# Kernel tuning notes

Measured on AMD Instinct MI355X. Metric: run time of the kernel, lower is better.

The kernel has to match this reference:

```python
import jax, jax.numpy as jnp
import numpy as np

HOLE_P = 0.05      # fraction of NaN (invalid) pixels
N_PROP = 8         # fixed propagation iterations for hole filling
DOWN_LIMIT = 512   # original code downsamples masks when max dim > 512

# cv2.getStructuringElement(cv2.MORPH_ELLIPSE, (3,3)) is the 4-neighbor cross
_CROSS = np.array([[0., 1., 0.], [1., 1., 1.], [0., 1., 0.]], np.float32)


def _conv_cross_hw(x):
    """3x3 cross conv on a single [H, W] map, zero padding."""
    k = jnp.asarray(_CROSS)[None, None]  # [1,1,3,3]
    y = jax.lax.conv_general_dilated(x[None, None], k, (1, 1), 'SAME',
                                     dimension_numbers=('NCHW', 'OIHW', 'NCHW'))
    return y[0, 0]


def _conv_cross_chw(x):
    """Depthwise 3x3 cross conv on [C, H, W], zero padding."""
    c = x.shape[0]
    k = jnp.tile(jnp.asarray(_CROSS)[None, None], (c, 1, 1, 1))  # [C,1,3,3]
    y = jax.lax.conv_general_dilated(x[None], k, (1, 1), 'SAME',
                                     feature_group_count=c,
                                     dimension_numbers=('NCHW', 'OIHW', 'NCHW'))
    return y[0]


def _dilated_union_mask(invalid_f):
    """Replicates the tri-branch: F.conv2d with weight [1,C,3,3] sums over
    channels (union of per-class invalid masks), then clamps to [0,1].
    When max dim > 512 it nearest-downsamples by dr, dilates, and nearest-
    upsamples back. invalid_f: [C,H,W] float -> [H,W] float in {0,1}."""
    c, h, w = invalid_f.shape
    s = invalid_f.sum(0)  # channel sum == conv over channel dim
    m = max(c, h, w)
    if m > DOWN_LIMIT:
        dr = m / DOWN_LIMIT
        hs, ws = int(h / dr), int(w / dr)
        # nearest downsample: index floor(i * h / hs)
        ri = (jnp.arange(hs) * h // hs).astype(jnp.int32)
        ci = (jnp.arange(ws) * w // ws).astype(jnp.int32)
        s_small = s[ri][:, ci]
        d_small = jnp.clip(_conv_cross_hw(s_small), 0.0, 1.0)
        # nearest upsample back to (h, w)
        ri_up = (jnp.arange(h) * hs // h).astype(jnp.int32)
        ci_up = (jnp.arange(w) * ws // w).astype(jnp.int32)
        d = d_small[ri_up][:, ci_up]
    else:
        d = jnp.clip(_conv_cross_hw(s), 0.0, 1.0)
    return d


def _fill_missing(x, invalid):
    """NaN-free formulation of fillMissingValues_tensor (tri mode).
    x: [C,H,W] float values; invalid: [C,H,W] bool (pixels that were NaN).
    Source pixels = valid pixels adjacent to the dilated union invalid mask
    (plus the 4 image corners, as in the original corner fixup). Invalid
    pixels are filled by iterative 4-neighbor weighted propagation from the
    source set (GPU-native stand-in for the Interp2D triangulated fill)."""
    invalid_f = invalid.astype(jnp.float32)
    dil = _dilated_union_mask(invalid_f)                       # [H,W]
    src = (dil[None] * (1.0 - invalid_f))                      # [C,H,W]
    # corner fixup: *0 then +1 -> forced to 1
    for (i, j) in [(0, 0), (0, -1), (-1, 0), (-1, -1)]:
        src = src.at[:, i, j].set(1.0)
    v = jnp.where(src > 0, jnp.where(invalid, 0.0, x), 0.0)
    w = jnp.where(src > 0, 1.0, 0.0)

    def step(carry, _):
        v, w = carry
        nv = _conv_cross_chw(v)
        nw = _conv_cross_chw(w)
        new = (w == 0.0) & (nw > 0.0)
        v = jnp.where(new, nv / jnp.maximum(nw, 1e-6), v)
        w = jnp.where(new, 1.0, w)
        return (v, w), None

    (v, w), _ = jax.lax.scan(step, (v, w), None, length=N_PROP)
    # replace only the invalid pixels (original keeps valid pixels untouched)
    return jnp.where(invalid, v, x)


def setup_inputs() -> dict:
    key = jax.random.key(0)
    k1, k2 = jax.random.split(key)
    x = jax.random.normal(k1, (16, 1024, 1024), dtype=jnp.float32)
    hole_u = jax.random.uniform(k2, (16, 1024, 1024), dtype=jnp.float32)
    return {"x": x, "hole_u": hole_u}


def reference(x, hole_u):
    invalid = hole_u < HOLE_P  # models torch.isnan(target_for_interp)
    return _fill_missing(x, invalid)
```

## Files before the change

### kernel.cpp

```cpp
#include <hip/hip_runtime.h>

#define HOLE_P 0.05f
#define TW 64
#define TH 64
#define HALO 8
#define PRW 88
#define PRH 82
#define PLN 7216
#define PWORDS 1804
#define QCAP 1536

__global__ void k_mask(const float* __restrict__ hole_u, unsigned char* __restrict__ inv_mask) {
    int t = blockIdx.x * blockDim.x + threadIdx.x;
    const float* base = hole_u + (size_t)t * 8;
    float4 a = *reinterpret_cast<const float4*>(base);
    float4 b = *reinterpret_cast<const float4*>(base + 4);
    unsigned int m = (a.x < HOLE_P ? 1u : 0u)  | (a.y < HOLE_P ? 2u : 0u)  |
                     (a.z < HOLE_P ? 4u : 0u)  | (a.w < HOLE_P ? 8u : 0u)  |
                     (b.x < HOLE_P ? 16u : 0u) | (b.y < HOLE_P ? 32u : 0u) |
                     (b.z < HOLE_P ? 64u : 0u) | (b.w < HOLE_P ? 128u : 0u);
    inv_mask[t] = (unsigned char)m;
}

__global__ void k_us(const unsigned char* __restrict__ inv_mask, unsigned char* __restrict__ u_small) {
    int t = blockIdx.x * blockDim.x + threadIdx.x;
    int i  = t >> 7;
    int jb = t & 127;
    const unsigned char* p = inv_mask + (i << 8) + jb;
    unsigned int b = 0;
#pragma unroll
    for (int c = 0; c < 16; ++c) b |= p[c * 131072];
    unsigned int o = (b & 1u) | (((b >> 2) & 1u) << 8) | (((b >> 4) & 1u) << 16) | (((b >> 6) & 1u) << 24);
    *reinterpret_cast<unsigned int*>(u_small + i * 512 + jb * 4) = o;
}

__global__ void k_dil(const unsigned char* __restrict__ u_small, unsigned char* __restrict__ d_small) {
    int g = blockIdx.x * blockDim.x + threadIdx.x;
    int i = g >> 9, j = g & 511;
    unsigned char d = u_small[g];
    if (i > 0)   d |= u_small[g - 512];
    if (i < 511) d |= u_small[g + 512];
    if (j > 0)   d |= u_small[g - 1];
    if (j < 511) d |= u_small[g + 1];
    d_small[g] = d;
}

__device__ __forceinline__ void halo_map(int h, int& ly, int& lxg) {
    if (h < 160)      { ly = h / 20;                lxg = h - (h / 20) * 20; }
    else if (h < 320) { int t2 = h - 160; ly = 72 + t2 / 20; lxg = t2 - (t2 / 20) * 20; }
    else              { int t2 = h - 320; ly = 8 + (t2 >> 2); int q = t2 & 3; lxg = q < 2 ? q : q + 16; }
}

__device__ __forceinline__ unsigned int enc_w(unsigned int src, unsigned int nib) {
    return ((src * 0x204081u) & 0x01010101u) | (((nib * 0x204081u) & 0x01010101u) << 7);
}

__device__ __forceinline__ float rcp_cnt(int cn) {
    float lo = (cn == 1) ? 1.0f : 0.5f;
    float hi = (cn == 3) ? (1.0f / 3.0f) : 0.25f;
    return (cn <= 2) ? lo : hi;
}

__global__ __launch_bounds__(512, 4) void k_fill(
    const float* __restrict__ x, const unsigned char* __restrict__ inv_mask,
    const unsigned char* __restrict__ d_small, float* __restrict__ out)
{
    __shared__ __align__(16) float v[PLN];
    __shared__ unsigned int w32[PWORDS];
    __shared__ unsigned short q[QCAP];
    __shared__ int qn;
    __shared__ int chgf[8], pendf[8];
    unsigned char* w = (unsigned char*)w32;

    const int tid = threadIdx.x;
    const int c   = blockIdx.z;
    const int by0 = blockIdx.y * TH;
    const int bx0 = blockIdx.x * TW;
    const float* xc = x + c * 1048576;
    const unsigned char* mc = inv_mask + c * 131072;
    float* oc = out + c * 1048576;
    const bool cornerTile = ((blockIdx.x == 0) | (blockIdx.x == 15)) &
                            ((blockIdx.y == 0) | (blockIdx.y == 15));

    if (tid < 8) { chgf[tid] = 0; pendf[tid] = 0; }
    if (tid == 0) qn = 0;
    if (tid < 204) {
        int wi;
        if (tid < 22)      wi = tid;
        else if (tid < 44) wi = 81 * 22 + (tid - 22);
        else {
            int r = ((tid - 44) >> 1) + 1;
            wi = r * 22 + (((tid - 44) & 1) ? 21 : 0);
        }
        w32[wi] = 0x7f7f7f7fu;
    }
    __syncthreads();

    int r0  = tid >> 4, cg0 = tid & 15;
    int gy0 = by0 + r0,      gx0 = bx0 + cg0 * 4;
    int gy1 = by0 + r0 + 32;
    float4 xx0 = *reinterpret_cast<const float4*>(xc + gy0 * 1024 + gx0);
    float4 xx1 = *reinterpret_cast<const float4*>(xc + gy1 * 1024 + gx0);
    unsigned int mb0 = mc[(gy0 << 7) + (gx0 >> 3)];
    unsigned int mb1 = mc[(gy1 << 7) + (gx0 >> 3)];
    unsigned short dsA = *reinterpret_cast<const unsigned short*>(d_small + ((gy0 >> 1) << 9) + (gx0 >> 1));
    unsigned short dsB = *reinterpret_cast<const unsigned short*>(d_small + ((gy1 >> 1) << 9) + (gx0 >> 1));

    int aly, alxg, bly, blxg;
    halo_map(tid, aly, alxg);
    const bool hasB = (tid < 64);
    halo_map(hasB ? tid + 512 : 0, bly, blxg);
    int agy  = by0 - HALO + aly,  agx0 = bx0 - HALO + alxg * 4;
    int bgy  = by0 - HALO + bly,  bgx0 = bx0 - HALO + blxg * 4;
    bool ain = ((unsigned)agy < 1024u) & ((unsigned)agx0 < 1024u);
    bool bin = hasB & ((unsigned)bgy < 1024u) & ((unsigned)bgx0 < 1024u);
    float4 axx = make_float4(0.f, 0.f, 0.f, 0.f), bxx = axx;
    unsigned int amb = 0, bmb = 0; unsigned short ads = 0, bds = 0;
    if (ain) {
        int gi = agy * 1024 + agx0;
        axx = *reinterpret_cast<const float4*>(xc + gi);
        amb = mc[(agy << 7) + (agx0 >> 3)];
        ads = *reinterpret_cast<const unsigned short*>(d_small + ((agy >> 1) << 9) + (agx0 >> 1));
    }
    if (bin) {
        int gi = bgy * 1024 + bgx0;
        bxx = *reinterpret_cast<const float4*>(xc + gi);
        bmb = mc[(bgy << 7) + (bgx0 >> 3)];
        bds = *reinterpret_cast<const unsigned short*>(d_small + ((bgy >> 1) << 9) + (bgx0 >> 1));
    }

    unsigned int fN0, fN1, fNA = 0, fNB = 0;
    unsigned int iN0, iN1, iNA = 0, iNB = 0;
    int P0i0, P0i1, P0A, P0B;
    {
        unsigned int nib = (mb0 >> (gx0 & 7)) & 0xfu;
        unsigned int db = ((dsA & 0xffu) ? 0x3u : 0u) | ((dsA & 0xff00u) ? 0xcu : 0u);
        unsigned int src = db & ~nib & 0xfu;
        if (cornerTile && ((gy0 == 0) | (gy0 == 1023)))
            src |= (gx0 == 0 ? 1u : 0u) | (gx0 == 1020 ? 8u : 0u);
        P0i0 = (9 + r0) * PRW + 12 + cg0 * 4;
        *reinterpret_cast<float4*>(&v[P0i0]) = xx0;
        w32[P0i0 >> 2] = enc_w(src, nib);
        fN0 = ~src & 0xfu; iN0 = nib;
    }
    {
        unsigned int nib = (mb1 >> (gx0 & 7)) & 0xfu;
        unsigned int db = ((dsB & 0xffu) ? 0x3u : 0u) | ((dsB & 0xff00u) ? 0xcu : 0u);
        unsigned int src = db & ~nib & 0xfu;
        if (cornerTile && ((gy1 == 0) | (gy1 == 1023)))
            src |= (gx0 == 0 ? 1u : 0u) | (gx0 == 1020 ? 8u : 0u);
        P0i1 = (9 + r0 + 32) * PRW + 12 + cg0 * 4;
        *reinterpret_cast<float4*>(&v[P0i1]) = xx1;
        w32[P0i1 >> 2] = enc_w(src, nib);
        fN1 = ~src & 0xfu; iN1 = nib;
    }
    {
        P0A = (aly + 1) * PRW + 4 + alxg * 4;
        unsigned int ww = 0x7f7f7f7fu;
        if (ain) {
            unsigned int nib = (amb >> (agx0 & 7)) & 0xfu;
            unsigned int db = ((ads & 0xffu) ? 0x3u : 0u) | ((ads & 0xff00u) ? 0xcu : 0u);
            unsigned int src = db & ~nib & 0xfu;
            ww = enc_w(src, nib);
            fNA = ~src & 0xfu; iNA = nib;
        }
        *reinterpret_cast<float4*>(&v[P0A]) = axx;
        w32[P0A >> 2] = ww;
    }
    P0B = (bly + 1) * PRW + 4 + blxg * 4;
    if (hasB) {
        unsigned int ww = 0x7f7f7f7fu;
        if (bin) {
            unsigned int nib = (bmb >> (bgx0 & 7)) & 0xfu;
            unsigned int db = ((bds & 0xffu) ? 0x3u : 0u) | ((bds & 0xff00u) ? 0xcu : 0u);
            unsigned int src = db & ~nib & 0xfu;
            ww = enc_w(src, nib);
            fNB = ~src & 0xfu; iNB = nib;
        }
        *reinterpret_cast<float4*>(&v[P0B]) = bxx;
        w32[P0B >> 2] = ww;
    }

    int cnt = __popc(fN0) + __popc(fN1) + __popc(fNA) + __popc(fNB);
    int lane = tid & 63;
    int xsum = cnt;
#pragma unroll
    for (int d = 1; d < 64; d <<= 1) {
        int y = __shfl_up(xsum, d, 64);
        if (lane >= d) xsum += y;
    }
    int base = 0;
    if (lane == 63) base = atomicAdd(&qn, xsum);
    base = __shfl(base, 63, 64);
    int idx = base + (xsum - cnt);
#define PUSH(m_, iv_, pd_, gp_) { unsigned int m = (m_); while (m) {            \
        int b = __builtin_ctz(m); m &= m - 1;                                   \
        unsigned int e = (unsigned int)((gp_) + b) | ((((iv_) >> b) & 1u) << 14)\
                         | ((((pd_) >> b) & 1u) << 15);                         \
        if (idx < QCAP) q[idx] = (unsigned short)e; ++idx; } }
    PUSH(fN0, iN0, fN0 & iN0, P0i0)
    PUSH(fN1, iN1, fN1 & iN1, P0i1)
    PUSH(fNA, iNA, 0u, P0A)
    PUSH(fNB, iNB, 0u, P0B)
#undef PUSH
    __syncthreads();

    if (cornerTile) {
        if (tid == 0) {
            int gy = (blockIdx.y == 0) ? 0 : 1023;
            int gx = (blockIdx.x == 0) ? 0 : 1023;
            int p = (9 + (gy - by0)) * PRW + 12 + (gx - bx0);
            if ((mc[(gy << 7) + (gx >> 3)] >> (gx & 7)) & 1u) v[p] = 0.0f;
        }
        __syncthreads();
    }

    const int n = qn;
    if (n <= QCAP) {
        for (int it = 0; it < 8; ++it) {
            int chg = 0, pend = 0;
            unsigned int thr = (unsigned int)it;
            for (int i = tid; i < n; i += 512) {
                unsigned int e = q[i];
                int p = e & 0x1fffu;
                if (w[p] & 0x7fu) continue;
                unsigned int qu = w[p - PRW] & 0x7fu;
                unsigned int qd = w[p + PRW] & 0x7fu;
                unsigned int ql = w[p - 1]   & 0x7fu;
                unsigned int qr = w[p + 1]   & 0x7fu;
                bool su = (qu - 1u) <= thr, sd = (qd - 1u) <= thr;
                bool sl = (ql - 1u) <= thr, sr = (qr - 1u) <= thr;
                float s = (su ? v[p - PRW] : 0.0f) + (sd ? v[p + PRW] : 0.0f)
                        + (sl ? v[p - 1]   : 0.0f) + (sr ? v[p + 1]   : 0.0f);
                int cn = (int)su + (int)sd + (int)sl + (int)sr;
                if (cn > 0) {
                    v[p] = s * rcp_cnt(cn);
                    w[p] = (unsigned char)((((e >> 14) & 1u) << 7) | (unsigned int)(it + 2));
                    chg = 1;
                } else {
                    pend |= (int)((e >> 15) & 1u);
                }
            }
            if (chg)  chgf[it] = 1;
            if (pend) pendf[it] = 1;
            __syncthreads();
            if (chgf[it] == 0 || pendf[it] == 0) break;
        }
    } else {
        for (int it = 0; it < 8; ++it) {
            int chg = 0;
            unsigned int thr = (unsigned int)it;
            for (int wp = tid; wp < PWORDS; wp += 512) {
                unsigned int cw = w32[wp];
                unsigned int st = cw & 0x7f7f7f7fu;
                if ((((st - 0x01010101u) & ~st) & 0x80808080u) == 0u) continue;
                int p0 = wp * 4;
#pragma unroll
                for (int b = 0; b < 4; ++b) {
                    if (((st >> (8 * b)) & 0x7fu) != 0u) continue;
                    int p = p0 + b;
                    unsigned int qu = w[p - PRW] & 0x7fu, qd = w[p + PRW] & 0x7fu;
                    unsigned int ql = w[p - 1] & 0x7fu,   qr = w[p + 1] & 0x7fu;
                    bool su = (qu - 1u) <= thr, sd = (qd - 1u) <= thr;
                    bool sl = (ql - 1u) <= thr, sr = (qr - 1u) <= thr;
                    float s = (su ? v[p - PRW] : 0.0f) + (sd ? v[p + PRW] : 0.0f)
                            + (sl ? v[p - 1]   : 0.0f) + (sr ? v[p + 1]   : 0.0f);
                    int cn = (int)su + (int)sd + (int)sl + (int)sr;
                    if (cn > 0) {
                        v[p] = s * rcp_cnt(cn);
                        w[p] = (unsigned char)(((cw >> (8 * b)) & 0x80u) | (unsigned int)(it + 2));
                        chg = 1;
                    }
                }
            }
            if (chg) chgf[it] = 1;
            __syncthreads();
            if (chgf[it] == 0) break;
        }
    }

#pragma unroll
    for (int k = 0; k < 2; ++k) {
        int r  = r0 + k * 32;
        int p0 = (9 + r) * PRW + 12 + cg0 * 4;
        unsigned int cw = w32[p0 >> 2];
        float4 vv = *reinterpret_cast<const float4*>(&v[p0]);
        float4 xx = (k == 0) ? xx0 : xx1;
        float4 o;
        o.x = (cw & 0x00000080u) ? vv.x : xx.x;
        o.y = (cw & 0x00008000u) ? vv.y : xx.y;
        o.z = (cw & 0x00800000u) ? vv.z : xx.z;
        o.w = (cw & 0x80000000u) ? vv.w : xx.w;
        *reinterpret_cast<float4*>(oc + (by0 + r) * 1024 + bx0 + cg0 * 4) = o;
    }
}

extern "C" void kernel_launch(void* const* d_in, const int* in_sizes, int n_in,
                              void* d_out, int out_size, void* d_ws, size_t ws_size,
                              hipStream_t stream) {
    (void)in_sizes; (void)n_in; (void)out_size; (void)ws_size;
    const float* x      = (const float*)d_in[0];
    const float* hole_u = (const float*)d_in[1];
    float* out = (float*)d_out;
    unsigned char* u_small  = (unsigned char*)d_ws;
    unsigned char* d_small  = u_small + 262144;
    unsigned char* inv_mask = d_small + 262144;

    k_mask<<<8192, 256, 0, stream>>>(hole_u, inv_mask);
    k_us  <<<256, 256, 0, stream>>>(inv_mask, u_small);
    k_dil <<<1024, 256, 0, stream>>>(u_small, d_small);
    dim3 grid(16, 16, 16);
    k_fill<<<grid, 512, 0, stream>>>(x, inv_mask, d_small, out);
}
```

Baseline: 54.14 us.

## Process two channels per fill block, prefetching second channel during first

Each k_fill block now handles two channels (c and c+8), so the grid is halved. The second channel's global loads are issued right after the first tile is encoded into shared memory, which lets them overlap the first channel's propagation. Setup work (halo maps, d_small decode, corner flags) is computed once and shared by both channels, and launch bounds go from 4 to 8 waves/blocks per SIMD hint. The costs are more registers held live across the first channel's work and fewer blocks in flight to hide latency.

```diff
diff --git a/kernel.cpp b/kernel.cpp
--- a/kernel.cpp
+++ b/kernel.cpp
@@ -61,7 +61,77 @@
     return (cn <= 2) ? lo : hi;
 }
 
-__global__ __launch_bounds__(512, 4) void k_fill(
+__device__ __forceinline__ void wl_jacobi(
+    float* v, unsigned char* w, const unsigned short* q, int n,
+    int* chgf, int* pendf, int tid)
+{
+    for (int it = 0; it < 8; ++it) {
+        int chg = 0, pend = 0;
+        unsigned int thr = (unsigned int)it;
+        for (int i = tid; i < n; i += 512) {
+            unsigned int e = q[i];
+            int p = e & 0x1fffu;
+            if (w[p] & 0x7fu) continue;
+            unsigned int qu = w[p - PRW] & 0x7fu;
+            unsigned int qd = w[p + PRW] & 0x7fu;
+            unsigned int ql = w[p - 1]   & 0x7fu;
+            unsigned int qr = w[p + 1]   & 0x7fu;
+            bool su = (qu - 1u) <= thr, sd = (qd - 1u) <= thr;
+            bool sl = (ql - 1u) <= thr, sr = (qr - 1u) <= thr;
+            float s = (su ? v[p - PRW] : 0.0f) + (sd ? v[p + PRW] : 0.0f)
+                    + (sl ? v[p - 1]   : 0.0f) + (sr ? v[p + 1]   : 0.0f);
+            int cn = (int)su + (int)sd + (int)sl + (int)sr;
+            if (cn > 0) {
+                v[p] = s * rcp_cnt(cn);
+                w[p] = (unsigned char)((((e >> 14) & 1u) << 7) | (unsigned int)(it + 2));
+                chg = 1;
+            } else {
+                pend |= (int)((e >> 15) & 1u);
+            }
+        }
+        if (chg)  chgf[it] = 1;
+        if (pend) pendf[it] = 1;
+        __syncthreads();
+        if (chgf[it] == 0 || pendf[it] == 0) break;
+    }
+}
+
+__device__ __forceinline__ void dense_sweep(
+    float* v, unsigned char* w, unsigned int* w32, int* chgf, int tid)
+{
+    for (int it = 0; it < 8; ++it) {
+        int chg = 0;
+        unsigned int thr = (unsigned int)it;
+        for (int wp = tid; wp < PWORDS; wp += 512) {
+            unsigned int cw = w32[wp];
+            unsigned int st = cw & 0x7f7f7f7fu;
+            if ((((st - 0x01010101u) & ~st) & 0x80808080u) == 0u) continue;
+            int p0 = wp * 4;
+#pragma unroll
+            for (int b = 0; b < 4; ++b) {
+                if (((st >> (8 * b)) & 0x7fu) != 0u) continue;
+                int p = p0 + b;
+                unsigned int qu = w[p - PRW] & 0x7fu, qd = w[p + PRW] & 0x7fu;
+                unsigned int ql = w[p - 1] & 0x7fu,   qr = w[p + 1] & 0x7fu;
+                bool su = (qu - 1u) <= thr, sd = (qd - 1u) <= thr;
+                bool sl = (ql - 1u) <= thr, sr = (qr - 1u) <= thr;
+                float s = (su ? v[p - PRW] : 0.0f) + (sd ? v[p + PRW] : 0.0f)
+                        + (sl ? v[p - 1]   : 0.0f) + (sr ? v[p + 1]   : 0.0f);
+                int cn = (int)su + (int)sd + (int)sl + (int)sr;
+                if (cn > 0) {
+                    v[p] = s * rcp_cnt(cn);
+                    w[p] = (unsigned char)(((cw >> (8 * b)) & 0x80u) | (unsigned int)(it + 2));
+                    chg = 1;
+                }
+            }
+        }
+        if (chg) chgf[it] = 1;
+        __syncthreads();
+        if (chgf[it] == 0) break;
+    }
+}
+
+__global__ __launch_bounds__(512, 8) void k_fill(
     const float* __restrict__ x, const unsigned char* __restrict__ inv_mask,
     const unsigned char* __restrict__ d_small, float* __restrict__ out)
 {
@@ -73,14 +143,59 @@
     unsigned char* w = (unsigned char*)w32;
 
     const int tid = threadIdx.x;
-    const int c   = blockIdx.z;
-    const int by0 = blockIdx.y * TH;
-    const int bx0 = blockIdx.x * TW;
-    const float* xc = x + c * 1048576;
-    const unsigned char* mc = inv_mask + c * 131072;
-    float* oc = out + c * 1048576;
-    const bool cornerTile = ((blockIdx.x == 0) | (blockIdx.x == 15)) &
-                            ((blockIdx.y == 0) | (blockIdx.y == 15));
+    const int lane = tid & 63;
+    const int tx = blockIdx.x, ty = blockIdx.y;
+    const int cA = blockIdx.z;
+    const int by0 = ty * TH, bx0 = tx * TW;
+    const bool cornerTile = ((tx == 0) | (tx == 15)) & ((ty == 0) | (ty == 15));
+
+    const float* xcA = x + cA * 1048576;
+    const float* xcB = xcA + 8 * 1048576;
+    const unsigned char* mcA = inv_mask + cA * 131072;
+    const unsigned char* mcB = mcA + 8 * 131072;
+    float* ocA = out + cA * 1048576;
+    float* ocB = ocA + 8 * 1048576;
+
+    const int r0 = tid >> 4, cg0 = tid & 15;
+    const int gy0 = by0 + r0, gx0 = bx0 + cg0 * 4, gy1 = gy0 + 32;
+    const int gi0 = gy0 * 1024 + gx0, gi1 = gy1 * 1024 + gx0;
+    const int mi0 = (gy0 << 7) + (gx0 >> 3), mi1 = (gy1 << 7) + (gx0 >> 3);
+    int aly, alxg, bly, blxg;
+    halo_map(tid, aly, alxg);
+    const bool hasB = (tid < 64);
+    halo_map(hasB ? tid + 512 : 0, bly, blxg);
+    const int agy = by0 - HALO + aly, agx0 = bx0 - HALO + alxg * 4;
+    const int bgy = by0 - HALO + bly, bgx0 = bx0 - HALO + blxg * 4;
+    const bool ain = ((unsigned)agy < 1024u) & ((unsigned)agx0 < 1024u);
+    const bool bin = hasB & ((unsigned)bgy < 1024u) & ((unsigned)bgx0 < 1024u);
+    const int giA = agy * 1024 + agx0, miA = (agy << 7) + (agx0 >> 3), diA = ((agy >> 1) << 9) + (agx0 >> 1);
+    const int giB = bgy * 1024 + bgx0, miB = (bgy << 7) + (bgx0 >> 3), diB = ((bgy >> 1) << 9) + (bgx0 >> 1);
+    const int P0i0 = (9 + r0) * PRW + 12 + cg0 * 4;
+    const int P0i1 = P0i0 + 32 * PRW;
+    const int P0A = (aly + 1) * PRW + 4 + alxg * 4;
+    const int P0B = (bly + 1) * PRW + 4 + blxg * 4;
+
+    float4 z4 = make_float4(0.f, 0.f, 0.f, 0.f);
+    float4 xx0A = *reinterpret_cast<const float4*>(xcA + gi0);
+    float4 xx1A = *reinterpret_cast<const float4*>(xcA + gi1);
+    float4 axxA = z4, bxxA = z4;
+    if (ain) axxA = *reinterpret_cast<const float4*>(xcA + giA);
+    if (bin) bxxA = *reinterpret_cast<const float4*>(xcA + giB);
+    unsigned int mb0A = mcA[mi0], mb1A = mcA[mi1];
+    unsigned int ambA = ain ? mcA[miA] : 0u;
+    unsigned int bmbA = bin ? mcA[miB] : 0u;
+    unsigned int ds0 = *reinterpret_cast<const unsigned short*>(d_small + ((gy0 >> 1) << 9) + (gx0 >> 1));
+    unsigned int ds1 = *reinterpret_cast<const unsigned short*>(d_small + ((gy1 >> 1) << 9) + (gx0 >> 1));
+    unsigned int dsa = ain ? *reinterpret_cast<const unsigned short*>(d_small + diA) : 0u;
+    unsigned int dsb = bin ? *reinterpret_cast<const unsigned short*>(d_small + diB) : 0u;
+    const unsigned int db0 = ((ds0 & 0xffu) ? 0x3u : 0u) | ((ds0 & 0xff00u) ? 0xcu : 0u);
+    const unsigned int db1 = ((ds1 & 0xffu) ? 0x3u : 0u) | ((ds1 & 0xff00u) ? 0xcu : 0u);
+    const unsigned int dbA = ((dsa & 0xffu) ? 0x3u : 0u) | ((dsa & 0xff00u) ? 0xcu : 0u);
+    const unsigned int dbB = ((dsb & 0xffu) ? 0x3u : 0u) | ((dsb & 0xff00u) ? 0xcu : 0u);
+    const unsigned int crn0 = (cornerTile && ((gy0 == 0) | (gy0 == 1023)))
+                              ? ((gx0 == 0 ? 1u : 0u) | (gx0 == 1020 ? 8u : 0u)) : 0u;
+    const unsigned int crn1 = (cornerTile && ((gy1 == 0) | (gy1 == 1023)))
+                              ? ((gx0 == 0 ? 1u : 0u) | (gx0 == 1020 ? 8u : 0u)) : 0u;
 
     if (tid < 8) { chgf[tid] = 0; pendf[tid] = 0; }
     if (tid == 0) qn = 0;
@@ -88,211 +203,130 @@
         int wi;
         if (tid < 22)      wi = tid;
         else if (tid < 44) wi = 81 * 22 + (tid - 22);
-        else {
-            int r = ((tid - 44) >> 1) + 1;
-            wi = r * 22 + (((tid - 44) & 1) ? 21 : 0);
-        }
+        else { int r = ((tid - 44) >> 1) + 1; wi = r * 22 + (((tid - 44) & 1) ? 21 : 0); }
         w32[wi] = 0x7f7f7f7fu;
     }
     __syncthreads();
 
-    int r0  = tid >> 4, cg0 = tid & 15;
-    int gy0 = by0 + r0,      gx0 = bx0 + cg0 * 4;
-    int gy1 = by0 + r0 + 32;
-    float4 xx0 = *reinterpret_cast<const float4*>(xc + gy0 * 1024 + gx0);
-    float4 xx1 = *reinterpret_cast<const float4*>(xc + gy1 * 1024 + gx0);
-    unsigned int mb0 = mc[(gy0 << 7) + (gx0 >> 3)];
-    unsigned int mb1 = mc[(gy1 << 7) + (gx0 >> 3)];
-    unsigned short dsA = *reinterpret_cast<const unsigned short*>(d_small + ((gy0 >> 1) << 9) + (gx0 >> 1));
-    unsigned short dsB = *reinterpret_cast<const unsigned short*>(d_small + ((gy1 >> 1) << 9) + (gx0 >> 1));
-
-    int aly, alxg, bly, blxg;
-    halo_map(tid, aly, alxg);
-    const bool hasB = (tid < 64);
-    halo_map(hasB ? tid + 512 : 0, bly, blxg);
-    int agy  = by0 - HALO + aly,  agx0 = bx0 - HALO + alxg * 4;
-    int bgy  = by0 - HALO + bly,  bgx0 = bx0 - HALO + blxg * 4;
-    bool ain = ((unsigned)agy < 1024u) & ((unsigned)agx0 < 1024u);
-    bool bin = hasB & ((unsigned)bgy < 1024u) & ((unsigned)bgx0 < 1024u);
-    float4 axx = make_float4(0.f, 0.f, 0.f, 0.f), bxx = axx;
-    unsigned int amb = 0, bmb = 0; unsigned short ads = 0, bds = 0;
-    if (ain) {
-        int gi = agy * 1024 + agx0;
-        axx = *reinterpret_cast<const float4*>(xc + gi);
-        amb = mc[(agy << 7) + (agx0 >> 3)];
-        ads = *reinterpret_cast<const unsigned short*>(d_small + ((agy >> 1) << 9) + (agx0 >> 1));
-    }
-    if (bin) {
-        int gi = bgy * 1024 + bgx0;
-        bxx = *reinterpret_cast<const float4*>(xc + gi);
-        bmb = mc[(bgy << 7) + (bgx0 >> 3)];
-        bds = *reinterpret_cast<const unsigned short*>(d_small + ((bgy >> 1) << 9) + (bgx0 >> 1));
-    }
-
-    unsigned int fN0, fN1, fNA = 0, fNB = 0;
-    unsigned int iN0, iN1, iNA = 0, iNB = 0;
-    int P0i0, P0i1, P0A, P0B;
+    float4 xx0B, xx1B, axxB = z4, bxxB = z4;
+    unsigned int mb0B, mb1B, ambB = 0u, bmbB = 0u;
+
+#define ENCODE_TILE(MB0, MB1, AMB, BMB, XX0, XX1, AXX, BXX)                       \
+    unsigned int fN0, fN1, fNA = 0, fNB = 0;                                      \
+    unsigned int iN0, iN1, iNA = 0, iNB = 0;                                      \
+    {                                                                             \
+        unsigned int nib = ((MB0) >> (gx0 & 7)) & 0xfu;                           \
+        unsigned int src = (db0 & ~nib & 0xfu) | crn0;                            \
+        *reinterpret_cast<float4*>(&v[P0i0]) = (XX0);                             \
+        w32[P0i0 >> 2] = enc_w(src, nib);                                         \
+        fN0 = ~src & 0xfu; iN0 = nib;                                             \
+    }                                                                             \
+    {                                                                             \
+        unsigned int nib = ((MB1) >> (gx0 & 7)) & 0xfu;                           \
+        unsigned int src = (db1 & ~nib & 0xfu) | crn1;                            \
+        *reinterpret_cast<float4*>(&v[P0i1]) = (XX1);                             \
+        w32[P0i1 >> 2] = enc_w(src, nib);                                         \
+        fN1 = ~src & 0xfu; iN1 = nib;                                             \
+    }                                                                             \
+    {                                                                             \
+        unsigned int ww = 0x7f7f7f7fu;                                            \
+        if (ain) {                                                                \
+            unsigned int nib = ((AMB) >> (agx0 & 7)) & 0xfu;                      \
+            unsigned int src = dbA & ~nib & 0xfu;                                 \
+            ww = enc_w(src, nib);                                                 \
+            fNA = ~src & 0xfu; iNA = nib;                                         \
+        }                                                                         \
+        *reinterpret_cast<float4*>(&v[P0A]) = (AXX);                              \
+        w32[P0A >> 2] = ww;                                                       \
+    }                                                                             \
+    if (hasB) {                                                                   \
+        unsigned int ww = 0x7f7f7f7fu;                                            \
+        if (bin) {                                                                \
+            unsigned int nib = ((BMB) >> (bgx0 & 7)) & 0xfu;                      \
+            unsigned int src = dbB & ~nib & 0xfu;                                 \
+            ww = enc_w(src, nib);                                                 \
+            fNB = ~src & 0xfu; iNB = nib;                                         \
+        }                                                                         \
+        *reinterpret_cast<float4*>(&v[P0B]) = (BXX);                              \
+        w32[P0B >> 2] = ww;                                                       \
+    }
+
+#define BUILD_RUN_STORE(MC, OC, XX0, XX1)                                         \
+    {                                                                             \
+        int cnt = __popc(fN0) + __popc(fN1) + __popc(fNA) + __popc(fNB);          \
+        int xsum = cnt;                                                           \
+        _Pragma("unroll")                                                         \
+        for (int d = 1; d < 64; d <<= 1) {                                        \
+            int y = __shfl_up(xsum, d, 64);                                       \
+            if (lane >= d) xsum += y;                                             \
+        }                                                                         \
+        int base = 0;                                                             \
+        if (lane == 63) base = atomicAdd(&qn, xsum);                              \
+        base = __shfl(base, 63, 64);                                              \
+        int idx = base + (xsum - cnt);                                            \
+        PUSH(fN0, iN0, fN0 & iN0, P0i0)                                           \
+        PUSH(fN1, iN1, fN1 & iN1, P0i1)                                           \
+        PUSH(fNA, iNA, 0u, P0A)                                                   \
+        PUSH(fNB, iNB, 0u, P0B)                                                   \
+        __syncthreads();                                                          \
+        if (cornerTile) {                                                         \
+            if (tid == 0) {                                                       \
+                int gy = (ty == 0) ? 0 : 1023;                                    \
+                int gx = (tx == 0) ? 0 : 1023;                                    \
+                int p = (9 + (gy - by0)) * PRW + 12 + (gx - bx0);                 \
+                if (((MC)[(gy << 7) + (gx >> 3)] >> (gx & 7)) & 1u) v[p] = 0.0f;  \
+            }                                                                     \
+            __syncthreads();                                                      \
+        }                                                                         \
+        const int n = qn;                                                         \
+        if (n <= QCAP) wl_jacobi(v, w, q, n, chgf, pendf, tid);                   \
+        else           dense_sweep(v, w, w32, chgf, tid);                         \
+        _Pragma("unroll")                                                         \
+        for (int k = 0; k < 2; ++k) {                                             \
+            int r  = r0 + k * 32;                                                 \
+            int p0 = (9 + r) * PRW + 12 + cg0 * 4;                                \
+            unsigned int cw = w32[p0 >> 2];                                       \
+            float4 vv = *reinterpret_cast<const float4*>(&v[p0]);                 \
+            float4 xx = (k == 0) ? (XX0) : (XX1);                                 \
+            float4 o;                                                             \
+            o.x = (cw & 0x00000080u) ? vv.x : xx.x;                               \
+            o.y = (cw & 0x00008000u) ? vv.y : xx.y;                               \
+            o.z = (cw & 0x00800000u) ? vv.z : xx.z;                               \
+            o.w = (cw & 0x80000000u) ? vv.w : xx.w;                               \
+            *reinterpret_cast<float4*>((OC) + (by0 + r) * 1024 + bx0 + cg0 * 4) = o; \
+        }                                                                         \
+    }
+
+#define PUSH(m_, iv_, pd_, gp_) { unsigned int m = (m_); while (m) {              \
+        int b = __builtin_ctz(m); m &= m - 1;                                     \
+        unsigned int e = (unsigned int)((gp_) + b) | ((((iv_) >> b) & 1u) << 14)  \
+                         | ((((pd_) >> b) & 1u) << 15);                           \
+        if (idx < QCAP) q[idx] = (unsigned short)e; ++idx; } }
+
     {
-        unsigned int nib = (mb0 >> (gx0 & 7)) & 0xfu;
-        unsigned int db = ((dsA & 0xffu) ? 0x3u : 0u) | ((dsA & 0xff00u) ? 0xcu : 0u);
-        unsigned int src = db & ~nib & 0xfu;
-        if (cornerTile && ((gy0 == 0) | (gy0 == 1023)))
-            src |= (gx0 == 0 ? 1u : 0u) | (gx0 == 1020 ? 8u : 0u);
-        P0i0 = (9 + r0) * PRW + 12 + cg0 * 4;
-        *reinterpret_cast<float4*>(&v[P0i0]) = xx0;
-        w32[P0i0 >> 2] = enc_w(src, nib);
-        fN0 = ~src & 0xfu; iN0 = nib;
-    }
+        ENCODE_TILE(mb0A, mb1A, ambA, bmbA, xx0A, xx1A, axxA, bxxA)
+        xx0B = *reinterpret_cast<const float4*>(xcB + gi0);
+        xx1B = *reinterpret_cast<const float4*>(xcB + gi1);
+        if (ain) axxB = *reinterpret_cast<const float4*>(xcB + giA);
+        if (bin) bxxB = *reinterpret_cast<const float4*>(xcB + giB);
+        mb0B = mcB[mi0]; mb1B = mcB[mi1];
+        if (ain) ambB = mcB[miA];
+        if (bin) bmbB = mcB[miB];
+        BUILD_RUN_STORE(mcA, ocA, xx0A, xx1A)
+    }
+
+    __syncthreads();
+    if (tid < 8) { chgf[tid] = 0; pendf[tid] = 0; }
+    if (tid == 0) qn = 0;
+    __syncthreads();
+
     {
-        unsigned int nib = (mb1 >> (gx0 & 7)) & 0xfu;
-        unsigned int db = ((dsB & 0xffu) ? 0x3u : 0u) | ((dsB & 0xff00u) ? 0xcu : 0u);
-        unsigned int src = db & ~nib & 0xfu;
-        if (cornerTile && ((gy1 == 0) | (gy1 == 1023)))
-            src |= (gx0 == 0 ? 1u : 0u) | (gx0 == 1020 ? 8u : 0u);
-        P0i1 = (9 + r0 + 32) * PRW + 12 + cg0 * 4;
-        *reinterpret_cast<float4*>(&v[P0i1]) = xx1;
-        w32[P0i1 >> 2] = enc_w(src, nib);
-        fN1 = ~src & 0xfu; iN1 = nib;
-    }
-    {
-        P0A = (aly + 1) * PRW + 4 + alxg * 4;
-        unsigned int ww = 0x7f7f7f7fu;
-        if (ain) {
-            unsigned int nib = (amb >> (agx0 & 7)) & 0xfu;
-            unsigned int db = ((ads & 0xffu) ? 0x3u : 0u) | ((ads & 0xff00u) ? 0xcu : 0u);
-            unsigned int src = db & ~nib & 0xfu;
-            ww = enc_w(src, nib);
-            fNA = ~src & 0xfu; iNA = nib;
-        }
-        *reinterpret_cast<float4*>(&v[P0A]) = axx;
-        w32[P0A >> 2] = ww;
-    }
-    P0B = (bly + 1) * PRW + 4 + blxg * 4;
-    if (hasB) {
-        unsigned int ww = 0x7f7f7f7fu;
-        if (bin) {
-            unsigned int nib = (bmb >> (bgx0 & 7)) & 0xfu;
-            unsigned int db = ((bds & 0xffu) ? 0x3u : 0u) | ((bds & 0xff00u) ? 0xcu : 0u);
-            unsigned int src = db & ~nib & 0xfu;
-            ww = enc_w(src, nib);
-            fNB = ~src & 0xfu; iNB = nib;
-        }
-        *reinterpret_cast<float4*>(&v[P0B]) = bxx;
-        w32[P0B >> 2] = ww;
-    }
-
-    int cnt = __popc(fN0) + __popc(fN1) + __popc(fNA) + __popc(fNB);
-    int lane = tid & 63;
-    int xsum = cnt;
-#pragma unroll
-    for (int d = 1; d < 64; d <<= 1) {
-        int y = __shfl_up(xsum, d, 64);
-        if (lane >= d) xsum += y;
-    }
-    int base = 0;
-    if (lane == 63) base = atomicAdd(&qn, xsum);
-    base = __shfl(base, 63, 64);
-    int idx = base + (xsum - cnt);
-#define PUSH(m_, iv_, pd_, gp_) { unsigned int m = (m_); while (m) {            \
-        int b = __builtin_ctz(m); m &= m - 1;                                   \
-        unsigned int e = (unsigned int)((gp_) + b) | ((((iv_) >> b) & 1u) << 14)\
-                         | ((((pd_) >> b) & 1u) << 15);                         \
-        if (idx < QCAP) q[idx] = (unsigned short)e; ++idx; } }
-    PUSH(fN0, iN0, fN0 & iN0, P0i0)
-    PUSH(fN1, iN1, fN1 & iN1, P0i1)
-    PUSH(fNA, iNA, 0u, P0A)
-    PUSH(fNB, iNB, 0u, P0B)
+        ENCODE_TILE(mb0B, mb1B, ambB, bmbB, xx0B, xx1B, axxB, bxxB)
+        BUILD_RUN_STORE(mcB, ocB, xx0B, xx1B)
+    }
 #undef PUSH
-    __syncthreads();
-
-    if (cornerTile) {
-        if (tid == 0) {
-            int gy = (blockIdx.y == 0) ? 0 : 1023;
-            int gx = (blockIdx.x == 0) ? 0 : 1023;
-            int p = (9 + (gy - by0)) * PRW + 12 + (gx - bx0);
-            if ((mc[(gy << 7) + (gx >> 3)] >> (gx & 7)) & 1u) v[p] = 0.0f;
-        }
-        __syncthreads();
-    }
-
-    const int n = qn;
-    if (n <= QCAP) {
-        for (int it = 0; it < 8; ++it) {
-            int chg = 0, pend = 0;
-            unsigned int thr = (unsigned int)it;
-            for (int i = tid; i < n; i += 512) {
-                unsigned int e = q[i];
-                int p = e & 0x1fffu;
-                if (w[p] & 0x7fu) continue;
-                unsigned int qu = w[p - PRW] & 0x7fu;
-                unsigned int qd = w[p + PRW] & 0x7fu;
-                unsigned int ql = w[p - 1]   & 0x7fu;
-                unsigned int qr = w[p + 1]   & 0x7fu;
-                bool su = (qu - 1u) <= thr, sd = (qd - 1u) <= thr;
-                bool sl = (ql - 1u) <= thr, sr = (qr - 1u) <= thr;
-                float s = (su ? v[p - PRW] : 0.0f) + (sd ? v[p + PRW] : 0.0f)
-                        + (sl ? v[p - 1]   : 0.0f) + (sr ? v[p + 1]   : 0.0f);
-                int cn = (int)su + (int)sd + (int)sl + (int)sr;
-                if (cn > 0) {
-                    v[p] = s * rcp_cnt(cn);
-                    w[p] = (unsigned char)((((e >> 14) & 1u) << 7) | (unsigned int)(it + 2));
-                    chg = 1;
-                } else {
-                    pend |= (int)((e >> 15) & 1u);
-                }
-            }
-            if (chg)  chgf[it] = 1;
-            if (pend) pendf[it] = 1;
-            __syncthreads();
-            if (chgf[it] == 0 || pendf[it] == 0) break;
-        }
-    } else {
-        for (int it = 0; it < 8; ++it) {
-            int chg = 0;
-            unsigned int thr = (unsigned int)it;
-            for (int wp = tid; wp < PWORDS; wp += 512) {
-                unsigned int cw = w32[wp];
-                unsigned int st = cw & 0x7f7f7f7fu;
-                if ((((st - 0x01010101u) & ~st) & 0x80808080u) == 0u) continue;
-                int p0 = wp * 4;
-#pragma unroll
-                for (int b = 0; b < 4; ++b) {
-                    if (((st >> (8 * b)) & 0x7fu) != 0u) continue;
-                    int p = p0 + b;
-                    unsigned int qu = w[p - PRW] & 0x7fu, qd = w[p + PRW] & 0x7fu;
-                    unsigned int ql = w[p - 1] & 0x7fu,   qr = w[p + 1] & 0x7fu;
-                    bool su = (qu - 1u) <= thr, sd = (qd - 1u) <= thr;
-                    bool sl = (ql - 1u) <= thr, sr = (qr - 1u) <= thr;
-                    float s = (su ? v[p - PRW] : 0.0f) + (sd ? v[p + PRW] : 0.0f)
-                            + (sl ? v[p - 1]   : 0.0f) + (sr ? v[p + 1]   : 0.0f);
-                    int cn = (int)su + (int)sd + (int)sl + (int)sr;
-                    if (cn > 0) {
-                        v[p] = s * rcp_cnt(cn);
-                        w[p] = (unsigned char)(((cw >> (8 * b)) & 0x80u) | (unsigned int)(it + 2));
-                        chg = 1;
-                    }
-                }
-            }
-            if (chg) chgf[it] = 1;
-            __syncthreads();
-            if (chgf[it] == 0) break;
-        }
-    }
-
-#pragma unroll
-    for (int k = 0; k < 2; ++k) {
-        int r  = r0 + k * 32;
-        int p0 = (9 + r) * PRW + 12 + cg0 * 4;
-        unsigned int cw = w32[p0 >> 2];
-        float4 vv = *reinterpret_cast<const float4*>(&v[p0]);
-        float4 xx = (k == 0) ? xx0 : xx1;
-        float4 o;
-        o.x = (cw & 0x00000080u) ? vv.x : xx.x;
-        o.y = (cw & 0x00008000u) ? vv.y : xx.y;
-        o.z = (cw & 0x00800000u) ? vv.z : xx.z;
-        o.w = (cw & 0x80000000u) ? vv.w : xx.w;
-        *reinterpret_cast<float4*>(oc + (by0 + r) * 1024 + bx0 + cg0 * 4) = o;
-    }
+#undef BUILD_RUN_STORE
+#undef ENCODE_TILE
 }
 
 extern "C" void kernel_launch(void* const* d_in, const int* in_sizes, int n_in,
@@ -309,6 +343,6 @@
     k_mask<<<8192, 256, 0, stream>>>(hole_u, inv_mask);
     k_us  <<<256, 256, 0, stream>>>(inv_mask, u_small);
     k_dil <<<1024, 256, 0, stream>>>(u_small, d_small);
-    dim3 grid(16, 16, 16);
+    dim3 grid(16, 16, 8);
     k_fill<<<grid, 512, 0, stream>>>(x, inv_mask, d_small, out);
 }
```

Result: slower. 69.71 us (+28.8%).
